# Kernel tuning notes

Measured on AMD Instinct MI355X. Metric: run time of the kernel, lower is better.

## Reference

```python
import jax, jax.numpy as jnp
import numpy as np

NF, NM, E = 100000, 20000, 1000000
H, FIN, MIN = 128, 8, 5


def setup_inputs() -> dict:
    key = jax.random.key(0)
    ks = jax.random.split(key, 32)

    def w(k, out_d, in_d):
        return jax.random.normal(k, (out_d, in_d), jnp.float32) / np.sqrt(in_d).astype(np.float32)

    inp = {}
    inp["x_fund"] = jax.random.normal(ks[0], (NF, FIN), jnp.float32)
    inp["x_manager"] = jax.random.normal(ks[1], (NM, MIN), jnp.float32)
    inp["fm_src"] = jax.random.randint(ks[2], (E,), 0, NF, jnp.int32)
    inp["fm_dst"] = jax.random.randint(ks[3], (E,), 0, NM, jnp.int32)
    # input projections
    inp["Wf"] = w(ks[4], H, FIN); inp["bf"] = jnp.zeros((H,), jnp.float32)
    inp["Wm"] = w(ks[5], H, MIN); inp["bm"] = jnp.zeros((H,), jnp.float32)
    # SAGEConv params per layer/relation: lin_l (neighbor, with bias), lin_r (root, no bias)
    i = 6
    for l in range(2):
        for rel in ("fm", "mf"):
            inp[f"Wl_{rel}{l}"] = w(ks[i], H, H); i += 1
            inp[f"bl_{rel}{l}"] = jnp.zeros((H,), jnp.float32)
            inp[f"Wr_{rel}{l}"] = w(ks[i], H, H); i += 1
    # classifier MLP (dropout is identity at inference)
    inp["Wc1"] = w(ks[i], H // 2, H); inp["bc1"] = jnp.zeros((H // 2,), jnp.float32); i += 1
    inp["Wc2"] = w(ks[i], 2, H // 2); inp["bc2"] = jnp.zeros((2,), jnp.float32)
    return inp


def _sage(x_src, x_dst, src, dst, Wl, bl, Wr, n_dst):
    # SAGEConv: lin_l(mean_{j in N(i)} x_j) + lin_r(x_i); mean of empty set -> 0
    msg = x_src[src]  # [E, H] gather
    agg = jax.ops.segment_sum(msg, dst, num_segments=n_dst)
    deg = jax.ops.segment_sum(jnp.ones_like(dst, dtype=x_src.dtype), dst, num_segments=n_dst)
    mean = agg / jnp.maximum(deg, 1.0)[:, None]
    return mean @ Wl.T + bl + x_dst @ Wr.T


def reference(x_fund, x_manager, fm_src, fm_dst, Wf, bf, Wm, bm,
              Wl_fm0, bl_fm0, Wr_fm0, Wl_mf0, bl_mf0, Wr_mf0,
              Wl_fm1, bl_fm1, Wr_fm1, Wl_mf1, bl_mf1, Wr_mf1,
              Wc1, bc1, Wc2, bc2):
    f = jax.nn.relu(x_fund @ Wf.T + bf)       # [NF, H]
    m = jax.nn.relu(x_manager @ Wm.T + bm)    # [NM, H]
    # layer 0: fund->manager and manager->fund (rev = transposed edges)
    m1 = jax.nn.relu(_sage(f, m, fm_src, fm_dst, Wl_fm0, bl_fm0, Wr_fm0, NM))
    f1 = jax.nn.relu(_sage(m, f, fm_dst, fm_src, Wl_mf0, bl_mf0, Wr_mf0, NF))
    # layer 1
    m2 = jax.nn.relu(_sage(f1, m1, fm_src, fm_dst, Wl_fm1, bl_fm1, Wr_fm1, NM))
    f2 = jax.nn.relu(_sage(m1, f1, fm_dst, fm_src, Wl_mf1, bl_mf1, Wr_mf1, NF))
    del m2
    # classifier on fund nodes (dropout=eval identity)
    h = jax.nn.relu(f2 @ Wc1.T + bc1)
    return h @ Wc2.T + bc2  # [NF, 2]
```

## Files before the change

kernel.cpp:

```cpp
#include <hip/hip_runtime.h>
#include <hip/hip_bf16.h>

#define HDIM 128
#define NG 8
#define NB 32

typedef unsigned short u16;
typedef unsigned int u32;
typedef __attribute__((ext_vector_type(8))) short bf16x8;
typedef __attribute__((ext_vector_type(4))) float f32x4;

__device__ __forceinline__ float bf2f(u16 u) {
  union { u32 i; float f; } x; x.i = ((u32)u) << 16; return x.f;
}
__device__ __forceinline__ u16 f2bf(float f) {
  union { float f; u32 i; } x; x.f = f;
  u32 r = x.i + 0x7fffu + ((x.i >> 16) & 1u);
  return (u16)(r >> 16);
}

static __device__ __forceinline__ int dmin(int a, int b) { return a < b ? a : b; }

__global__ __launch_bounds__(1024) void k_hist2(const int* __restrict__ src, const int* __restrict__ dst,
                                                int* __restrict__ cnt, int E, int NF, int NM) {
  __shared__ int h[15104];
  int g = blockIdx.x & (NG - 1);
  int c = blockIdx.x >> 3;
  int t = threadIdx.x;
  int NFg = (NF + NG - 1) / NG, NMg = (NM + NG - 1) / NG;
  int loF = g * NFg, hiF = dmin(NF, loF + NFg);
  int loM = g * NMg, hiM = dmin(NM, loM + NMg);
  int nb = NFg + NMg;
  for (int j = t; j < nb; j += 1024) h[j] = 0;
  __syncthreads();
  int Epc = (E + NB - 1) / NB;
  int c0 = c * Epc, c1 = dmin(E, c0 + Epc);
  for (int i = c0 + t; i < c1; i += 1024) {
    int s = src[i], d = dst[i];
    if (s >= loF && s < hiF) atomicAdd(&h[s - loF], 1);
    if (d >= loM && d < hiM) atomicAdd(&h[NFg + (d - loM)], 1);
  }
  __syncthreads();
  size_t K = (size_t)NF + NM;
  int* cc = cnt + (size_t)c * K;
  for (int j = t; j < NFg; j += 1024) {
    int k = loF + j;
    if (k < hiF) cc[k] = h[j];
  }
  for (int j = t; j < NMg; j += 1024) {
    int k = loM + j;
    if (k < hiM) cc[NF + k] = h[NFg + j];
  }
}

__global__ __launch_bounds__(256) void k_colscan(int* __restrict__ cnt, int* __restrict__ deg, int K) {
  int k = blockIdx.x * 256 + threadIdx.x;
  if (k >= K) return;
  int s = 0;
  #pragma unroll 4
  for (int c = 0; c < NB; ++c) {
    int* p = cnt + (size_t)c * K + k;
    int v = *p;
    *p = s;
    s += v;
  }
  deg[k] = s;
}

__global__ __launch_bounds__(256) void k_scan_chunks(const int* __restrict__ deg, int n,
                                                     int* __restrict__ rowptr, int* __restrict__ part) {
  __shared__ int sm[256];
  int t = threadIdx.x;
  int base = blockIdx.x * 1024 + t * 4;
  int v0 = 0, v1 = 0, v2 = 0, v3 = 0;
  if (base + 0 < n) v0 = deg[base + 0];
  if (base + 1 < n) v1 = deg[base + 1];
  if (base + 2 < n) v2 = deg[base + 2];
  if (base + 3 < n) v3 = deg[base + 3];
  int s = v0 + v1 + v2 + v3;
  sm[t] = s;
  __syncthreads();
  for (int off = 1; off < 256; off <<= 1) {
    int x = (t >= off) ? sm[t - off] : 0;
    __syncthreads();
    sm[t] += x;
    __syncthreads();
  }
  int excl = sm[t] - s;
  if (t == 255) part[blockIdx.x] = sm[255];
  if (base + 0 < n) rowptr[base + 0] = excl;
  if (base + 1 < n) rowptr[base + 1] = excl + v0;
  if (base + 2 < n) rowptr[base + 2] = excl + v0 + v1;
  if (base + 3 < n) rowptr[base + 3] = excl + v0 + v1 + v2;
}

__global__ __launch_bounds__(256) void k_scan_part(int* __restrict__ part, int nb) {
  __shared__ int sm[256];
  int t = threadIdx.x;
  int s = (t < nb) ? part[t] : 0;
  sm[t] = s;
  __syncthreads();
  for (int off = 1; off < 256; off <<= 1) {
    int x = (t >= off) ? sm[t - off] : 0;
    __syncthreads();
    sm[t] += x;
    __syncthreads();
  }
  if (t < nb) part[t] = sm[t] - s;
}

__global__ __launch_bounds__(256) void k_add_off(int* __restrict__ rowptr, const int* __restrict__ part,
                                                 int n, int total) {
  int i = blockIdx.x * 256 + threadIdx.x;
  int s = gridDim.x * 256;
  for (; i < n; i += s) rowptr[i] += part[i >> 10];
  if (blockIdx.x == 0 && threadIdx.x == 0) rowptr[n] = total;
}

__global__ __launch_bounds__(1024) void k_scatter2(const int* __restrict__ src, const int* __restrict__ dst,
                                                   const int* __restrict__ rp_f, const int* __restrict__ rp_m,
                                                   const int* __restrict__ cnt,
                                                   int* __restrict__ col_f, int* __restrict__ col_m,
                                                   int E, int NF, int NM) {
  __shared__ int cur[15104];
  int g = blockIdx.x & (NG - 1);
  int c = blockIdx.x >> 3;
  int t = threadIdx.x;
  int NFg = (NF + NG - 1) / NG, NMg = (NM + NG - 1) / NG;
  int loF = g * NFg, hiF = dmin(NF, loF + NFg);
  int loM = g * NMg, hiM = dmin(NM, loM + NMg);
  size_t K = (size_t)NF + NM;
  const int* cc = cnt + (size_t)c * K;
  for (int j = t; j < NFg; j += 1024) {
    int k = loF + j;
    if (k < hiF) cur[j] = rp_f[k] + cc[k];
  }
  for (int j = t; j < NMg; j += 1024) {
    int k = loM + j;
    if (k < hiM) cur[NFg + j] = rp_m[k] + cc[NF + k];
  }
  __syncthreads();
  int Epc = (E + NB - 1) / NB;
  int c0 = c * Epc, c1 = dmin(E, c0 + Epc);
  for (int i = c0 + t; i < c1; i += 1024) {
    int s = src[i], d = dst[i];
    if (s >= loF && s < hiF) {
      int p = atomicAdd(&cur[s - loF], 1);
      col_f[p] = d;
    }
    if (d >= loM && d < hiM) {
      int p = atomicAdd(&cur[NFg + (d - loM)], 1);
      col_m[p] = s;
    }
  }
}

__global__ __launch_bounds__(256) void k_w2bf(const float* __restrict__ s0, const float* __restrict__ s1,
                                              const float* __restrict__ s2, const float* __restrict__ s3,
                                              const float* __restrict__ s4, const float* __restrict__ s5,
                                              const float* __restrict__ s6, u16* __restrict__ dst) {
  int i = blockIdx.x * 256 + threadIdx.x;
  const float* s; int off = i;
  if (i < 16384) { s = s0; }
  else if (i < 32768) { s = s1; off = i - 16384; }
  else if (i < 49152) { s = s2; off = i - 32768; }
  else if (i < 65536) { s = s3; off = i - 49152; }
  else if (i < 81920) { s = s4; off = i - 65536; }
  else if (i < 98304) { s = s5; off = i - 81920; }
  else { s = s6; off = i - 98304; }
  dst[i] = f2bf(s[off]);
}

__global__ __launch_bounds__(256) void k_proj(const float* __restrict__ x, const float* __restrict__ W,
                                              const float* __restrict__ b, u16* __restrict__ out,
                                              int n, int din) {
  __shared__ float Wls[128 * 9];
  __shared__ float bs[128];
  int t = threadIdx.x;
  int sw = din | 1;
  for (int i = t; i < 128 * din; i += 256) {
    int c = i / din, k = i - c * din;
    Wls[c * sw + k] = W[i];
  }
  for (int i = t; i < 128; i += 256) bs[i] = b[i];
  __syncthreads();
  int idx = blockIdx.x * 256 + t;
  int gs = gridDim.x * 256;
  for (; idx < n * 64; idx += gs) {
    int row = idx >> 6, cp = (idx & 63) * 2;
    float a0 = bs[cp], a1 = bs[cp + 1];
    const float* xr = x + (size_t)row * din;
    for (int k = 0; k < din; ++k) {
      float xv = xr[k];
      a0 += Wls[cp * sw + k] * xv;
      a1 += Wls[(cp + 1) * sw + k] * xv;
    }
    a0 = fmaxf(a0, 0.f);
    a1 = fmaxf(a1, 0.f);
    u32 pk = (u32)f2bf(a0) | ((u32)f2bf(a1) << 16);
    *(u32*)(out + (size_t)row * HDIM + cp) = pk;
  }
}

__global__ __launch_bounds__(256) void k_agg2(const u16* __restrict__ feat, const int* __restrict__ rowptr,
                                              const int* __restrict__ col, u16* __restrict__ out, int ndst) {
  int t = threadIdx.x;
  int grp = t >> 4, lc = t & 15;
  int nd = blockIdx.x * 16 + grp;
  if (nd >= ndst) return;
  int s0 = rowptr[nd], s1 = rowptr[nd + 1];
  float a0=0.f,a1=0.f,a2=0.f,a3=0.f,a4=0.f,a5=0.f,a6=0.f,a7=0.f;
  const u16* fb = feat + lc * 8;
  int j = s0;
  for (; j + 3 < s1; j += 4) {
    uint4 v0 = *(const uint4*)(fb + (size_t)col[j]     * HDIM);
    uint4 v1 = *(const uint4*)(fb + (size_t)col[j + 1] * HDIM);
    uint4 v2 = *(const uint4*)(fb + (size_t)col[j + 2] * HDIM);
    uint4 v3 = *(const uint4*)(fb + (size_t)col[j + 3] * HDIM);
    a0 += bf2f((u16)v0.x) + bf2f((u16)v1.x) + bf2f((u16)v2.x) + bf2f((u16)v3.x);
    a1 += bf2f((u16)(v0.x>>16)) + bf2f((u16)(v1.x>>16)) + bf2f((u16)(v2.x>>16)) + bf2f((u16)(v3.x>>16));
    a2 += bf2f((u16)v0.y) + bf2f((u16)v1.y) + bf2f((u16)v2.y) + bf2f((u16)v3.y);
    a3 += bf2f((u16)(v0.y>>16)) + bf2f((u16)(v1.y>>16)) + bf2f((u16)(v2.y>>16)) + bf2f((u16)(v3.y>>16));
    a4 += bf2f((u16)v0.z) + bf2f((u16)v1.z) + bf2f((u16)v2.z) + bf2f((u16)v3.z);
    a5 += bf2f((u16)(v0.z>>16)) + bf2f((u16)(v1.z>>16)) + bf2f((u16)(v2.z>>16)) + bf2f((u16)(v3.z>>16));
    a6 += bf2f((u16)v0.w) + bf2f((u16)v1.w) + bf2f((u16)v2.w) + bf2f((u16)v3.w);
    a7 += bf2f((u16)(v0.w>>16)) + bf2f((u16)(v1.w>>16)) + bf2f((u16)(v2.w>>16)) + bf2f((u16)(v3.w>>16));
  }
  for (; j < s1; ++j) {
    uint4 v = *(const uint4*)(fb + (size_t)col[j] * HDIM);
    a0 += bf2f((u16)v.x); a1 += bf2f((u16)(v.x >> 16));
    a2 += bf2f((u16)v.y); a3 += bf2f((u16)(v.y >> 16));
    a4 += bf2f((u16)v.z); a5 += bf2f((u16)(v.z >> 16));
    a6 += bf2f((u16)v.w); a7 += bf2f((u16)(v.w >> 16));
  }
  float inv = (s1 > s0) ? 1.f / (float)(s1 - s0) : 0.f;
  uint4 pk;
  pk.x = (u32)f2bf(a0 * inv) | ((u32)f2bf(a1 * inv) << 16);
  pk.y = (u32)f2bf(a2 * inv) | ((u32)f2bf(a3 * inv) << 16);
  pk.z = (u32)f2bf(a4 * inv) | ((u32)f2bf(a5 * inv) << 16);
  pk.w = (u32)f2bf(a6 * inv) | ((u32)f2bf(a7 * inv) << 16);
  *(uint4*)(out + (size_t)nd * HDIM + lc * 8) = pk;
}

__global__ __launch_bounds__(256) void k_ling(const u16* __restrict__ X1, const u16* __restrict__ W1,
                                              const u16* __restrict__ X2, const u16* __restrict__ W2,
                                              const u16* __restrict__ ADD, const float* __restrict__ bias,
                                              u16* __restrict__ out, int n, int do_relu) {
  int t = threadIdx.x;
  int w = t >> 6, lane = t & 63;
  int lm = lane & 15, lk = (lane >> 4) * 8;
  int cg = (lane >> 4) * 4;
  int row0 = blockIdx.x * 128 + w * 32;
  if (row0 >= n) return;
  int r0 = row0 + lm;       if (r0 >= n) r0 = n - 1;
  int r1 = row0 + 16 + lm;  if (r1 >= n) r1 = n - 1;
  f32x4 acc0[8], acc1[8];
  #pragma unroll
  for (int i = 0; i < 8; ++i) { acc0[i] = (f32x4){0.f,0.f,0.f,0.f}; acc1[i] = (f32x4){0.f,0.f,0.f,0.f}; }
  const u16* Xp = X1;
  const u16* Wp = W1;
  for (int p = 0; p < 2; ++p) {
    #pragma unroll
    for (int ks = 0; ks < 4; ++ks) {
      bf16x8 b0 = *(const bf16x8*)(Xp + (size_t)r0 * 128 + ks * 32 + lk);
      bf16x8 b1 = *(const bf16x8*)(Xp + (size_t)r1 * 128 + ks * 32 + lk);
      #pragma unroll
      for (int nt = 0; nt < 8; ++nt) {
        bf16x8 a = *(const bf16x8*)(Wp + (size_t)(nt * 16 + lm) * 128 + ks * 32 + lk);
        acc0[nt] = __builtin_amdgcn_mfma_f32_16x16x32_bf16(a, b0, acc0[nt], 0, 0, 0);
        acc1[nt] = __builtin_amdgcn_mfma_f32_16x16x32_bf16(a, b1, acc1[nt], 0, 0, 0);
      }
    }
    if (!X2) break;
    Xp = X2;
    Wp = W2;
  }
  #pragma unroll
  for (int half = 0; half < 2; ++half) {
    int m = row0 + half * 16 + lm;
    if (m >= n) break;
    f32x4* acc = half ? acc1 : acc0;
    #pragma unroll
    for (int nt = 0; nt < 8; ++nt) {
      int c = nt * 16 + cg;
      float v0 = acc[nt][0], v1 = acc[nt][1], v2 = acc[nt][2], v3 = acc[nt][3];
      if (bias) {
        float4 bv = *(const float4*)(bias + c);
        v0 += bv.x; v1 += bv.y; v2 += bv.z; v3 += bv.w;
      }
      if (ADD) {
        ushort4 av = *(const ushort4*)(ADD + (size_t)m * 128 + c);
        v0 += bf2f(av.x); v1 += bf2f(av.y); v2 += bf2f(av.z); v3 += bf2f(av.w);
      }
      if (do_relu) {
        v0 = fmaxf(v0, 0.f); v1 = fmaxf(v1, 0.f); v2 = fmaxf(v2, 0.f); v3 = fmaxf(v3, 0.f);
      }
      ushort4 pk;
      pk.x = f2bf(v0); pk.y = f2bf(v1); pk.z = f2bf(v2); pk.w = f2bf(v3);
      *(ushort4*)(out + (size_t)m * 128 + c) = pk;
    }
  }
}

__global__ __launch_bounds__(256) void k_cls(const u16* __restrict__ f2, const u16* __restrict__ Wc1bf,
                                             const float* __restrict__ bc1, const float* __restrict__ Wc2,
                                             const float* __restrict__ bc2, float* __restrict__ out, int n) {
  int t = threadIdx.x;
  int w = t >> 6, lane = t & 63;
  int lm = lane & 15, lk = (lane >> 4) * 8;
  int cg = (lane >> 4) * 4;
  int row0 = blockIdx.x * 64 + w * 16;
  if (row0 >= n) return;
  int rB = row0 + lm;
  if (rB >= n) rB = n - 1;
  f32x4 acc[4];
  #pragma unroll
  for (int i = 0; i < 4; ++i) acc[i] = (f32x4){0.f, 0.f, 0.f, 0.f};
  #pragma unroll
  for (int ks = 0; ks < 4; ++ks) {
    bf16x8 b = *(const bf16x8*)(f2 + (size_t)rB * 128 + ks * 32 + lk);
    #pragma unroll
    for (int nt = 0; nt < 4; ++nt) {
      bf16x8 a = *(const bf16x8*)(Wc1bf + (size_t)(nt * 16 + lm) * 128 + ks * 32 + lk);
      acc[nt] = __builtin_amdgcn_mfma_f32_16x16x32_bf16(a, b, acc[nt], 0, 0, 0);
    }
  }
  float s0 = 0.f, s1 = 0.f;
  #pragma unroll
  for (int nt = 0; nt < 4; ++nt) {
    int k = nt * 16 + cg;
    float4 bv = *(const float4*)(bc1 + k);
    float4 w0 = *(const float4*)(Wc2 + k);
    float4 w1 = *(const float4*)(Wc2 + 64 + k);
    float h0 = fmaxf(acc[nt][0] + bv.x, 0.f);
    float h1 = fmaxf(acc[nt][1] + bv.y, 0.f);
    float h2 = fmaxf(acc[nt][2] + bv.z, 0.f);
    float h3 = fmaxf(acc[nt][3] + bv.w, 0.f);
    s0 += h0 * w0.x + h1 * w0.y + h2 * w0.z + h3 * w0.w;
    s1 += h0 * w1.x + h1 * w1.y + h2 * w1.z + h3 * w1.w;
  }
  s0 += __shfl_xor(s0, 16); s1 += __shfl_xor(s1, 16);
  s0 += __shfl_xor(s0, 32); s1 += __shfl_xor(s1, 32);
  int m = row0 + lm;
  if (lane < 16 && m < n) {
    out[(size_t)m * 2 + 0] = s0 + bc2[0];
    out[(size_t)m * 2 + 1] = s1 + bc2[1];
  }
}

static inline int imin(int a, int b) { return a < b ? a : b; }

extern "C" void kernel_launch(void* const* d_in, const int* in_sizes, int n_in,
                              void* d_out, int out_size, void* d_ws, size_t ws_size,
                              hipStream_t stream) {
  const float* x_fund = (const float*)d_in[0];
  const float* x_mgr  = (const float*)d_in[1];
  const int* fm_src   = (const int*)d_in[2];
  const int* fm_dst   = (const int*)d_in[3];
  const float* Wf = (const float*)d_in[4];
  const float* bfb = (const float*)d_in[5];
  const float* Wm = (const float*)d_in[6];
  const float* bm = (const float*)d_in[7];
  const float* Wl_fm0 = (const float*)d_in[8];
  const float* bl_fm0 = (const float*)d_in[9];
  const float* Wr_fm0 = (const float*)d_in[10];
  const float* Wl_mf0 = (const float*)d_in[11];
  const float* bl_mf0 = (const float*)d_in[12];
  const float* Wr_mf0 = (const float*)d_in[13];
  const float* Wl_mf1 = (const float*)d_in[17];
  const float* bl_mf1 = (const float*)d_in[18];
  const float* Wr_mf1 = (const float*)d_in[19];
  const float* Wc1 = (const float*)d_in[20];
  const float* bc1 = (const float*)d_in[21];
  const float* Wc2 = (const float*)d_in[22];
  const float* bc2 = (const float*)d_in[23];

  int NF = in_sizes[0] / 8;
  int NM = in_sizes[1] / 5;
  int E  = in_sizes[2];
  int K  = NF + NM;

  char* ws = (char*)d_ws;
  size_t off = 0;
  auto alloc = [&](size_t bytes) -> char* {
    char* p = ws + off;
    off += (bytes + 255) & ~(size_t)255;
    return p;
  };
  u16* f_b   = (u16*)alloc((size_t)NF * HDIM * 2);
  u16* f1_b  = (u16*)alloc((size_t)NF * HDIM * 2);
  u16* f2_b  = (u16*)alloc((size_t)NF * HDIM * 2);
  u16* aggf  = (u16*)alloc((size_t)NF * HDIM * 2);
  u16* m_b   = (u16*)alloc((size_t)NM * HDIM * 2);
  u16* m1_b  = (u16*)alloc((size_t)NM * HDIM * 2);
  u16* t_b   = (u16*)alloc((size_t)NM * HDIM * 2);
  u16* aggm  = (u16*)alloc((size_t)NM * HDIM * 2);
  u16* wbf   = (u16*)alloc((size_t)106496 * 2);
  int* rp_f  = (int*)alloc((size_t)(NF + 1) * 4);
  int* rp_m  = (int*)alloc((size_t)(NM + 1) * 4);
  int* deg   = (int*)alloc((size_t)K * 4);
  int* col_f = (int*)alloc((size_t)E * 4);
  int* col_m = (int*)alloc((size_t)E * 4);
  int* cnt   = (int*)alloc((size_t)NB * K * 4);
  int* part_f = (int*)alloc(256 * 4);
  int* part_m = (int*)alloc(256 * 4);
  (void)ws_size; (void)n_in; (void)out_size;

  u16* Wlfm0b = wbf + 0;
  u16* Wrfm0b = wbf + 16384;
  u16* Wlmf0b = wbf + 32768;
  u16* Wrmf0b = wbf + 49152;
  u16* Wlmf1b = wbf + 65536;
  u16* Wrmf1b = wbf + 81920;
  u16* Wc1b   = wbf + 98304;

  int nch_f = (NF + 1023) / 1024;
  int nch_m = (NM + 1023) / 1024;

  k_w2bf<<<416, 256, 0, stream>>>(Wl_fm0, Wr_fm0, Wl_mf0, Wr_mf0, Wl_mf1, Wr_mf1, Wc1, wbf);

  k_hist2<<<NG * NB, 1024, 0, stream>>>(fm_src, fm_dst, cnt, E, NF, NM);
  k_colscan<<<(K + 255) / 256, 256, 0, stream>>>(cnt, deg, K);
  k_scan_chunks<<<nch_f, 256, 0, stream>>>(deg, NF, rp_f, part_f);
  k_scan_chunks<<<nch_m, 256, 0, stream>>>(deg + NF, NM, rp_m, part_m);
  k_scan_part<<<1, 256, 0, stream>>>(part_f, nch_f);
  k_scan_part<<<1, 256, 0, stream>>>(part_m, nch_m);
  k_add_off<<<(NF + 255) / 256, 256, 0, stream>>>(rp_f, part_f, NF, E);
  k_add_off<<<(NM + 255) / 256, 256, 0, stream>>>(rp_m, part_m, NM, E);
  k_scatter2<<<NG * NB, 1024, 0, stream>>>(fm_src, fm_dst, rp_f, rp_m, cnt, col_f, col_m, E, NF, NM);

  k_proj<<<imin((NF * 64 + 255) / 256, 4096), 256, 0, stream>>>(x_fund, Wf, bfb, f_b, NF, 8);
  k_proj<<<imin((NM * 64 + 255) / 256, 4096), 256, 0, stream>>>(x_mgr, Wm, bm, m_b, NM, 5);

  k_agg2<<<(NM + 15) / 16, 256, 0, stream>>>(f_b, rp_m, col_m, aggm, NM);
  k_ling<<<(NM + 127) / 128, 256, 0, stream>>>(aggm, Wlfm0b, m_b, Wrfm0b, nullptr, bl_fm0, m1_b, NM, 1);

  k_ling<<<(NM + 127) / 128, 256, 0, stream>>>(m_b, Wlmf0b, nullptr, nullptr, nullptr, nullptr, t_b, NM, 0);
  k_agg2<<<(NF + 15) / 16, 256, 0, stream>>>(t_b, rp_f, col_f, aggf, NF);
  k_ling<<<(NF + 127) / 128, 256, 0, stream>>>(f_b, Wrmf0b, nullptr, nullptr, aggf, bl_mf0, f1_b, NF, 1);

  k_ling<<<(NM + 127) / 128, 256, 0, stream>>>(m1_b, Wlmf1b, nullptr, nullptr, nullptr, nullptr, t_b, NM, 0);
  k_agg2<<<(NF + 15) / 16, 256, 0, stream>>>(t_b, rp_f, col_f, aggf, NF);
  k_ling<<<(NF + 127) / 128, 256, 0, stream>>>(f1_b, Wrmf1b, nullptr, nullptr, aggf, bl_mf1, f2_b, NF, 1);

  k_cls<<<(NF + 63) / 64, 256, 0, stream>>>(f2_b, Wc1b, bc1, Wc2, bc2, (float*)d_out, NF);
}
```

Before: 324.7 us.

## Merge both layers' manager-to-fund aggregations into one 256-wide gather pass

Layer-1 fund aggregation depends only on m1, which is ready before layer 0's fund update. The change therefore projects m and m1 through their lin_l weights in one combined kernel into a 256-wide buffer, then gathers both halves over the fund CSR in a single pass. This removes one full traversal of the million-edge gather and one projection launch. It also fuses the paired scan, offset and input-projection kernels for funds and managers into single launches to cut launch overhead. In exchange the combined aggregate buffer doubles in size and k_ling gains stride parameters.

```diff
diff --git a/kernel.cpp b/kernel.cpp
--- a/kernel.cpp
+++ b/kernel.cpp
@@ -67,16 +67,23 @@
   deg[k] = s;
 }
 
-__global__ __launch_bounds__(256) void k_scan_chunks(const int* __restrict__ deg, int n,
-                                                     int* __restrict__ rowptr, int* __restrict__ part) {
+__global__ __launch_bounds__(256) void k_scan_chunks2(const int* __restrict__ deg, int NF, int NM,
+                                                      int nchf, int* __restrict__ rp_f, int* __restrict__ rp_m,
+                                                      int* __restrict__ part_f, int* __restrict__ part_m) {
   __shared__ int sm[256];
   int t = threadIdx.x;
-  int base = blockIdx.x * 1024 + t * 4;
+  bool isM = (int)blockIdx.x >= nchf;
+  int b = isM ? (blockIdx.x - nchf) : blockIdx.x;
+  const int* d = isM ? (deg + NF) : deg;
+  int n = isM ? NM : NF;
+  int* rowptr = isM ? rp_m : rp_f;
+  int* part = isM ? part_m : part_f;
+  int base = b * 1024 + t * 4;
   int v0 = 0, v1 = 0, v2 = 0, v3 = 0;
-  if (base + 0 < n) v0 = deg[base + 0];
-  if (base + 1 < n) v1 = deg[base + 1];
-  if (base + 2 < n) v2 = deg[base + 2];
-  if (base + 3 < n) v3 = deg[base + 3];
+  if (base + 0 < n) v0 = d[base + 0];
+  if (base + 1 < n) v1 = d[base + 1];
+  if (base + 2 < n) v2 = d[base + 2];
+  if (base + 3 < n) v3 = d[base + 3];
   int s = v0 + v1 + v2 + v3;
   sm[t] = s;
   __syncthreads();
@@ -87,16 +94,19 @@
     __syncthreads();
   }
   int excl = sm[t] - s;
-  if (t == 255) part[blockIdx.x] = sm[255];
+  if (t == 255) part[b] = sm[255];
   if (base + 0 < n) rowptr[base + 0] = excl;
   if (base + 1 < n) rowptr[base + 1] = excl + v0;
   if (base + 2 < n) rowptr[base + 2] = excl + v0 + v1;
   if (base + 3 < n) rowptr[base + 3] = excl + v0 + v1 + v2;
 }
 
-__global__ __launch_bounds__(256) void k_scan_part(int* __restrict__ part, int nb) {
+__global__ __launch_bounds__(256) void k_scan_part2(int* __restrict__ part_f, int nchf,
+                                                    int* __restrict__ part_m, int nchm) {
   __shared__ int sm[256];
   int t = threadIdx.x;
+  int* part = blockIdx.x ? part_m : part_f;
+  int nb = blockIdx.x ? nchm : nchf;
   int s = (t < nb) ? part[t] : 0;
   sm[t] = s;
   __syncthreads();
@@ -109,12 +119,17 @@
   if (t < nb) part[t] = sm[t] - s;
 }
 
-__global__ __launch_bounds__(256) void k_add_off(int* __restrict__ rowptr, const int* __restrict__ part,
-                                                 int n, int total) {
+__global__ __launch_bounds__(256) void k_add_off2(int* __restrict__ rp_f, const int* __restrict__ part_f, int NF,
+                                                  int* __restrict__ rp_m, const int* __restrict__ part_m, int NM,
+                                                  int total) {
   int i = blockIdx.x * 256 + threadIdx.x;
   int s = gridDim.x * 256;
-  for (; i < n; i += s) rowptr[i] += part[i >> 10];
-  if (blockIdx.x == 0 && threadIdx.x == 0) rowptr[n] = total;
+  int tot = NF + NM;
+  for (; i < tot; i += s) {
+    if (i < NF) rp_f[i] += part_f[i >> 10];
+    else { int j = i - NF; rp_m[j] += part_m[j >> 10]; }
+  }
+  if (blockIdx.x == 0 && threadIdx.x == 0) { rp_f[NF] = total; rp_m[NM] = total; }
 }
 
 __global__ __launch_bounds__(1024) void k_scatter2(const int* __restrict__ src, const int* __restrict__ dst,
@@ -171,34 +186,59 @@
   dst[i] = f2bf(s[off]);
 }
 
-__global__ __launch_bounds__(256) void k_proj(const float* __restrict__ x, const float* __restrict__ W,
-                                              const float* __restrict__ b, u16* __restrict__ out,
-                                              int n, int din) {
-  __shared__ float Wls[128 * 9];
-  __shared__ float bs[128];
-  int t = threadIdx.x;
-  int sw = din | 1;
-  for (int i = t; i < 128 * din; i += 256) {
-    int c = i / din, k = i - c * din;
-    Wls[c * sw + k] = W[i];
-  }
-  for (int i = t; i < 128; i += 256) bs[i] = b[i];
+__global__ __launch_bounds__(256) void k_proj2(const float* __restrict__ xf, const float* __restrict__ Wf,
+                                               const float* __restrict__ bfp, const float* __restrict__ xm,
+                                               const float* __restrict__ Wm, const float* __restrict__ bmp,
+                                               u16* __restrict__ outf, u16* __restrict__ outm,
+                                               int NF, int NM) {
+  __shared__ float Wfs[128 * 9];
+  __shared__ float Wms[128 * 5];
+  __shared__ float bsf[128];
+  __shared__ float bsm[128];
+  int t = threadIdx.x;
+  for (int i = t; i < 128 * 8; i += 256) {
+    int c = i >> 3, k = i & 7;
+    Wfs[c * 9 + k] = Wf[i];
+  }
+  for (int i = t; i < 128 * 5; i += 256) {
+    int c = i / 5, k = i - c * 5;
+    Wms[c * 5 + k] = Wm[i];
+  }
+  for (int i = t; i < 128; i += 256) { bsf[i] = bfp[i]; bsm[i] = bmp[i]; }
   __syncthreads();
+  int totF = NF * 64;
+  int tot = totF + NM * 64;
   int idx = blockIdx.x * 256 + t;
   int gs = gridDim.x * 256;
-  for (; idx < n * 64; idx += gs) {
-    int row = idx >> 6, cp = (idx & 63) * 2;
-    float a0 = bs[cp], a1 = bs[cp + 1];
-    const float* xr = x + (size_t)row * din;
-    for (int k = 0; k < din; ++k) {
-      float xv = xr[k];
-      a0 += Wls[cp * sw + k] * xv;
-      a1 += Wls[(cp + 1) * sw + k] * xv;
-    }
-    a0 = fmaxf(a0, 0.f);
-    a1 = fmaxf(a1, 0.f);
-    u32 pk = (u32)f2bf(a0) | ((u32)f2bf(a1) << 16);
-    *(u32*)(out + (size_t)row * HDIM + cp) = pk;
+  for (; idx < tot; idx += gs) {
+    if (idx < totF) {
+      int row = idx >> 6, cp = (idx & 63) * 2;
+      float a0 = bsf[cp], a1 = bsf[cp + 1];
+      const float* xr = xf + (size_t)row * 8;
+      #pragma unroll
+      for (int k = 0; k < 8; ++k) {
+        float xv = xr[k];
+        a0 += Wfs[cp * 9 + k] * xv;
+        a1 += Wfs[(cp + 1) * 9 + k] * xv;
+      }
+      a0 = fmaxf(a0, 0.f); a1 = fmaxf(a1, 0.f);
+      u32 pk = (u32)f2bf(a0) | ((u32)f2bf(a1) << 16);
+      *(u32*)(outf + (size_t)row * HDIM + cp) = pk;
+    } else {
+      int k2 = idx - totF;
+      int row = k2 >> 6, cp = (k2 & 63) * 2;
+      float a0 = bsm[cp], a1 = bsm[cp + 1];
+      const float* xr = xm + (size_t)row * 5;
+      #pragma unroll
+      for (int k = 0; k < 5; ++k) {
+        float xv = xr[k];
+        a0 += Wms[cp * 5 + k] * xv;
+        a1 += Wms[(cp + 1) * 5 + k] * xv;
+      }
+      a0 = fmaxf(a0, 0.f); a1 = fmaxf(a1, 0.f);
+      u32 pk = (u32)f2bf(a0) | ((u32)f2bf(a1) << 16);
+      *(u32*)(outm + (size_t)row * HDIM + cp) = pk;
+    }
   }
 }
 
@@ -242,10 +282,51 @@
   *(uint4*)(out + (size_t)nd * HDIM + lc * 8) = pk;
 }
 
+__global__ __launch_bounds__(256) void k_aggd(const u16* __restrict__ tc, const int* __restrict__ rowptr,
+                                              const int* __restrict__ col, u16* __restrict__ aggc, int ndst) {
+  int t = threadIdx.x;
+  int grp = t >> 5, lc = t & 31;
+  int nd = blockIdx.x * 8 + grp;
+  if (nd >= ndst) return;
+  int s0 = rowptr[nd], s1 = rowptr[nd + 1];
+  float a0=0.f,a1=0.f,a2=0.f,a3=0.f,a4=0.f,a5=0.f,a6=0.f,a7=0.f;
+  const u16* fb = tc + lc * 8;
+  int j = s0;
+  for (; j + 3 < s1; j += 4) {
+    uint4 v0 = *(const uint4*)(fb + (size_t)col[j]     * 256);
+    uint4 v1 = *(const uint4*)(fb + (size_t)col[j + 1] * 256);
+    uint4 v2 = *(const uint4*)(fb + (size_t)col[j + 2] * 256);
+    uint4 v3 = *(const uint4*)(fb + (size_t)col[j + 3] * 256);
+    a0 += bf2f((u16)v0.x) + bf2f((u16)v1.x) + bf2f((u16)v2.x) + bf2f((u16)v3.x);
+    a1 += bf2f((u16)(v0.x>>16)) + bf2f((u16)(v1.x>>16)) + bf2f((u16)(v2.x>>16)) + bf2f((u16)(v3.x>>16));
+    a2 += bf2f((u16)v0.y) + bf2f((u16)v1.y) + bf2f((u16)v2.y) + bf2f((u16)v3.y);
+    a3 += bf2f((u16)(v0.y>>16)) + bf2f((u16)(v1.y>>16)) + bf2f((u16)(v2.y>>16)) + bf2f((u16)(v3.y>>16));
+    a4 += bf2f((u16)v0.z) + bf2f((u16)v1.z) + bf2f((u16)v2.z) + bf2f((u16)v3.z);
+    a5 += bf2f((u16)(v0.z>>16)) + bf2f((u16)(v1.z>>16)) + bf2f((u16)(v2.z>>16)) + bf2f((u16)(v3.z>>16));
+    a6 += bf2f((u16)v0.w) + bf2f((u16)v1.w) + bf2f((u16)v2.w) + bf2f((u16)v3.w);
+    a7 += bf2f((u16)(v0.w>>16)) + bf2f((u16)(v1.w>>16)) + bf2f((u16)(v2.w>>16)) + bf2f((u16)(v3.w>>16));
+  }
+  for (; j < s1; ++j) {
+    uint4 v = *(const uint4*)(fb + (size_t)col[j] * 256);
+    a0 += bf2f((u16)v.x); a1 += bf2f((u16)(v.x >> 16));
+    a2 += bf2f((u16)v.y); a3 += bf2f((u16)(v.y >> 16));
+    a4 += bf2f((u16)v.z); a5 += bf2f((u16)(v.z >> 16));
+    a6 += bf2f((u16)v.w); a7 += bf2f((u16)(v.w >> 16));
+  }
+  float inv = (s1 > s0) ? 1.f / (float)(s1 - s0) : 0.f;
+  uint4 pk;
+  pk.x = (u32)f2bf(a0 * inv) | ((u32)f2bf(a1 * inv) << 16);
+  pk.y = (u32)f2bf(a2 * inv) | ((u32)f2bf(a3 * inv) << 16);
+  pk.z = (u32)f2bf(a4 * inv) | ((u32)f2bf(a5 * inv) << 16);
+  pk.w = (u32)f2bf(a6 * inv) | ((u32)f2bf(a7 * inv) << 16);
+  *(uint4*)(aggc + (size_t)nd * 256 + lc * 8) = pk;
+}
+
 __global__ __launch_bounds__(256) void k_ling(const u16* __restrict__ X1, const u16* __restrict__ W1,
                                               const u16* __restrict__ X2, const u16* __restrict__ W2,
                                               const u16* __restrict__ ADD, const float* __restrict__ bias,
-                                              u16* __restrict__ out, int n, int do_relu) {
+                                              u16* __restrict__ out, int n, int do_relu,
+                                              int ostride, int astride) {
   int t = threadIdx.x;
   int w = t >> 6, lane = t & 63;
   int lm = lane & 15, lk = (lane >> 4) * 8;
@@ -289,7 +370,7 @@
         v0 += bv.x; v1 += bv.y; v2 += bv.z; v3 += bv.w;
       }
       if (ADD) {
-        ushort4 av = *(const ushort4*)(ADD + (size_t)m * 128 + c);
+        ushort4 av = *(const ushort4*)(ADD + (size_t)m * astride + c);
         v0 += bf2f(av.x); v1 += bf2f(av.y); v2 += bf2f(av.z); v3 += bf2f(av.w);
       }
       if (do_relu) {
@@ -297,7 +378,54 @@
       }
       ushort4 pk;
       pk.x = f2bf(v0); pk.y = f2bf(v1); pk.z = f2bf(v2); pk.w = f2bf(v3);
-      *(ushort4*)(out + (size_t)m * 128 + c) = pk;
+      *(ushort4*)(out + (size_t)m * ostride + c) = pk;
+    }
+  }
+}
+
+__global__ __launch_bounds__(256) void k_ling2(const u16* __restrict__ XA, const u16* __restrict__ WA,
+                                               const u16* __restrict__ XB, const u16* __restrict__ WB,
+                                               u16* __restrict__ out, int n) {
+  int nb = gridDim.x >> 1;
+  bool second = (int)blockIdx.x >= nb;
+  const u16* X = second ? XB : XA;
+  const u16* W = second ? WB : WA;
+  int bid = second ? (blockIdx.x - nb) : blockIdx.x;
+  u16* o = out + (second ? 128 : 0);
+  int t = threadIdx.x;
+  int w = t >> 6, lane = t & 63;
+  int lm = lane & 15, lk = (lane >> 4) * 8;
+  int cg = (lane >> 4) * 4;
+  int row0 = bid * 128 + w * 32;
+  if (row0 >= n) return;
+  int r0 = row0 + lm;       if (r0 >= n) r0 = n - 1;
+  int r1 = row0 + 16 + lm;  if (r1 >= n) r1 = n - 1;
+  f32x4 acc0[8], acc1[8];
+  #pragma unroll
+  for (int i = 0; i < 8; ++i) { acc0[i] = (f32x4){0.f,0.f,0.f,0.f}; acc1[i] = (f32x4){0.f,0.f,0.f,0.f}; }
+  #pragma unroll
+  for (int ks = 0; ks < 4; ++ks) {
+    bf16x8 b0 = *(const bf16x8*)(X + (size_t)r0 * 128 + ks * 32 + lk);
+    bf16x8 b1 = *(const bf16x8*)(X + (size_t)r1 * 128 + ks * 32 + lk);
+    #pragma unroll
+    for (int nt = 0; nt < 8; ++nt) {
+      bf16x8 a = *(const bf16x8*)(W + (size_t)(nt * 16 + lm) * 128 + ks * 32 + lk);
+      acc0[nt] = __builtin_amdgcn_mfma_f32_16x16x32_bf16(a, b0, acc0[nt], 0, 0, 0);
+      acc1[nt] = __builtin_amdgcn_mfma_f32_16x16x32_bf16(a, b1, acc1[nt], 0, 0, 0);
+    }
+  }
+  #pragma unroll
+  for (int half = 0; half < 2; ++half) {
+    int m = row0 + half * 16 + lm;
+    if (m >= n) break;
+    f32x4* acc = half ? acc1 : acc0;
+    #pragma unroll
+    for (int nt = 0; nt < 8; ++nt) {
+      int c = nt * 16 + cg;
+      ushort4 pk;
+      pk.x = f2bf(acc[nt][0]); pk.y = f2bf(acc[nt][1]);
+      pk.z = f2bf(acc[nt][2]); pk.w = f2bf(acc[nt][3]);
+      *(ushort4*)(o + (size_t)m * 256 + c) = pk;
     }
   }
 }
@@ -390,10 +518,10 @@
   u16* f_b   = (u16*)alloc((size_t)NF * HDIM * 2);
   u16* f1_b  = (u16*)alloc((size_t)NF * HDIM * 2);
   u16* f2_b  = (u16*)alloc((size_t)NF * HDIM * 2);
-  u16* aggf  = (u16*)alloc((size_t)NF * HDIM * 2);
+  u16* aggc  = (u16*)alloc((size_t)NF * 256 * 2);
   u16* m_b   = (u16*)alloc((size_t)NM * HDIM * 2);
   u16* m1_b  = (u16*)alloc((size_t)NM * HDIM * 2);
-  u16* t_b   = (u16*)alloc((size_t)NM * HDIM * 2);
+  u16* tcomb = (u16*)alloc((size_t)NM * 256 * 2);
   u16* aggm  = (u16*)alloc((size_t)NM * HDIM * 2);
   u16* wbf   = (u16*)alloc((size_t)106496 * 2);
   int* rp_f  = (int*)alloc((size_t)(NF + 1) * 4);
@@ -421,27 +549,26 @@
 
   k_hist2<<<NG * NB, 1024, 0, stream>>>(fm_src, fm_dst, cnt, E, NF, NM);
   k_colscan<<<(K + 255) / 256, 256, 0, stream>>>(cnt, deg, K);
-  k_scan_chunks<<<nch_f, 256, 0, stream>>>(deg, NF, rp_f, part_f);
-  k_scan_chunks<<<nch_m, 256, 0, stream>>>(deg + NF, NM, rp_m, part_m);
-  k_scan_part<<<1, 256, 0, stream>>>(part_f, nch_f);
-  k_scan_part<<<1, 256, 0, stream>>>(part_m, nch_m);
-  k_add_off<<<(NF + 255) / 256, 256, 0, stream>>>(rp_f, part_f, NF, E);
-  k_add_off<<<(NM + 255) / 256, 256, 0, stream>>>(rp_m, part_m, NM, E);
+  k_scan_chunks2<<<nch_f + nch_m, 256, 0, stream>>>(deg, NF, NM, nch_f, rp_f, rp_m, part_f, part_m);
+  k_scan_part2<<<2, 256, 0, stream>>>(part_f, nch_f, part_m, nch_m);
+  k_add_off2<<<(K + 255) / 256, 256, 0, stream>>>(rp_f, part_f, NF, rp_m, part_m, NM, E);
   k_scatter2<<<NG * NB, 1024, 0, stream>>>(fm_src, fm_dst, rp_f, rp_m, cnt, col_f, col_m, E, NF, NM);
 
-  k_proj<<<imin((NF * 64 + 255) / 256, 4096), 256, 0, stream>>>(x_fund, Wf, bfb, f_b, NF, 8);
-  k_proj<<<imin((NM * 64 + 255) / 256, 4096), 256, 0, stream>>>(x_mgr, Wm, bm, m_b, NM, 5);
+  k_proj2<<<imin(((NF + NM) * 64 + 255) / 256, 4096), 256, 0, stream>>>(
+      x_fund, Wf, bfb, x_mgr, Wm, bm, f_b, m_b, NF, NM);
 
   k_agg2<<<(NM + 15) / 16, 256, 0, stream>>>(f_b, rp_m, col_m, aggm, NM);
-  k_ling<<<(NM + 127) / 128, 256, 0, stream>>>(aggm, Wlfm0b, m_b, Wrfm0b, nullptr, bl_fm0, m1_b, NM, 1);
-
-  k_ling<<<(NM + 127) / 128, 256, 0, stream>>>(m_b, Wlmf0b, nullptr, nullptr, nullptr, nullptr, t_b, NM, 0);
-  k_agg2<<<(NF + 15) / 16, 256, 0, stream>>>(t_b, rp_f, col_f, aggf, NF);
-  k_ling<<<(NF + 127) / 128, 256, 0, stream>>>(f_b, Wrmf0b, nullptr, nullptr, aggf, bl_mf0, f1_b, NF, 1);
-
-  k_ling<<<(NM + 127) / 128, 256, 0, stream>>>(m1_b, Wlmf1b, nullptr, nullptr, nullptr, nullptr, t_b, NM, 0);
-  k_agg2<<<(NF + 15) / 16, 256, 0, stream>>>(t_b, rp_f, col_f, aggf, NF);
-  k_ling<<<(NF + 127) / 128, 256, 0, stream>>>(f1_b, Wrmf1b, nullptr, nullptr, aggf, bl_mf1, f2_b, NF, 1);
+  k_ling<<<(NM + 127) / 128, 256, 0, stream>>>(aggm, Wlfm0b, m_b, Wrfm0b, nullptr, bl_fm0,
+                                               m1_b, NM, 1, 128, 128);
+
+  k_ling2<<<2 * ((NM + 127) / 128), 256, 0, stream>>>(m_b, Wlmf0b, m1_b, Wlmf1b, tcomb, NM);
+
+  k_aggd<<<(NF + 7) / 8, 256, 0, stream>>>(tcomb, rp_f, col_f, aggc, NF);
+
+  k_ling<<<(NF + 127) / 128, 256, 0, stream>>>(f_b, Wrmf0b, nullptr, nullptr, aggc, bl_mf0,
+                                               f1_b, NF, 1, 128, 256);
+  k_ling<<<(NF + 127) / 128, 256, 0, stream>>>(f1_b, Wrmf1b, nullptr, nullptr, aggc + 128, bl_mf1,
+                                               f2_b, NF, 1, 128, 256);
 
   k_cls<<<(NF + 63) / 64, 256, 0, stream>>>(f2_b, Wc1b, bc1, Wc2, bc2, (float*)d_out, NF);
 }
```

Measured after the change: 307.9 us. 1.05x faster.
